# Kernel tuning notes

Hardware: AMD Instinct MI355X
Metric: run time of the kernel (lower is better)

Reference implementation:

```python
import jax, jax.numpy as jnp
import numpy as np

PRUNING_THRESHOLD = 0.02


def setup_inputs() -> dict:
    key = jax.random.key(0)
    ks = jax.random.split(key, 9)
    B, T, D = 2, 2048, 512
    H, S = 8, 16
    hd = D // H
    x = jax.random.normal(ks[0], (B, T, D), dtype=jnp.float32)
    Wqkv = jax.random.normal(ks[1], (3 * D, D), dtype=jnp.float32) * 0.02
    Wout = jax.random.normal(ks[2], (D, D), dtype=jnp.float32) * 0.02
    splat_centers = jax.random.normal(ks[3], (H, S, hd), dtype=jnp.float32) * 0.3
    splat_deltas = jax.random.normal(ks[4], (H, S, hd), dtype=jnp.float32) * 0.05
    splat_log_scales = jax.random.normal(ks[5], (H, S), dtype=jnp.float32) * 0.2 + jnp.float32(np.log(0.5))
    splat_log_amplitudes = jax.random.normal(ks[6], (H, S), dtype=jnp.float32) * 0.1 - 0.5
    movement_scale = jnp.float32(0.08)
    temperature = jnp.float32(1.0)
    return {"x": x, "Wqkv": Wqkv, "Wout": Wout,
            "splat_centers": splat_centers, "splat_deltas": splat_deltas,
            "splat_log_scales": splat_log_scales, "splat_log_amplitudes": splat_log_amplitudes,
            "movement_scale": movement_scale, "temperature": temperature}


def reference(x, Wqkv, Wout, splat_centers, splat_deltas,
              splat_log_scales, splat_log_amplitudes, movement_scale, temperature):
    B, T, D = x.shape
    H, S, hd = splat_centers.shape
    # qkv projection (nn.Linear: y = x @ W.T), split into q,k,v per head
    qkv = (x @ Wqkv.T).reshape(B, T, 3, H, hd)
    q, k, v = qkv[:, :, 0], qkv[:, :, 1], qkv[:, :, 2]  # [B,T,H,hd]
    # effective centers with bounded movement (eval mode: no warmup)
    bounded_scale = jax.nn.sigmoid(movement_scale) * 0.2
    centers = splat_centers + splat_deltas * bounded_scale  # [H,S,hd]
    scales = jnp.clip(jnp.exp(splat_log_scales), 0.01, 2.0)  # [H,S]
    amplitudes = jnp.clip(jnp.exp(splat_log_amplitudes), 1e-06, 10.0)
    amplitudes = amplitudes * (amplitudes > PRUNING_THRESHOLD).astype(amplitudes.dtype)
    # squared distances from tokens to splat centers: [B,T,H,S]
    q_dists = jnp.sum((q[:, :, :, None, :] - centers[None, None]) ** 2, axis=-1)
    k_dists = jnp.sum((k[:, :, :, None, :] - centers[None, None]) ** 2, axis=-1)
    inv_var = 1.0 / (scales ** 2 + 1e-08)  # [H,S]
    q_w = jnp.exp(-0.5 * q_dists * inv_var)  # [B,T,H,S]
    k_w = jnp.exp(-0.5 * k_dists * inv_var)
    # per-head splat-weighted logits: [B,T(query i),T(key j),H]
    logits = jnp.einsum('bihs,bjhs,hs->bijh', q_w, k_w, amplitudes)
    temp = jnp.clip(temperature, 0.1, 10.0)
    # NOTE: original vectorized path softmaxes over dim=1 (query axis) -- faithful
    attn = jax.nn.softmax(logits / temp, axis=1)
    out = jnp.einsum('btjh,bjhd->bthd', attn, v).reshape(B, T, D)
    return out @ Wout.T
```

## Files before the change

### kernel.cpp

```cpp
#include <hip/hip_runtime.h>
#include <hip/hip_bf16.h>
#include <hip/hip_fp16.h>
#include <cstdint>
#include <cstddef>

#define T_SEQ 2048
#define NBATCH 2
#define DIMD 512
#define NH 8
#define NS 16
#define HD 64
#define NBH 16

using s16x8 = __attribute__((ext_vector_type(8))) short;
using f32x4 = __attribute__((ext_vector_type(4))) float;

static __device__ inline unsigned short f2bf(float f) {
  __hip_bfloat16 h = __float2bfloat16(f);
  return reinterpret_cast<unsigned short&>(h);
}
static __device__ inline unsigned short f2h(float f) {
  __half h = __float2half(f);
  return reinterpret_cast<unsigned short&>(h);
}
static __device__ inline float h2f(unsigned short u) {
  __half h = reinterpret_cast<__half&>(u);
  return __half2float(h);
}
static __device__ inline unsigned int pack2(float a, float b) {
  return (unsigned int)f2bf(a) | ((unsigned int)f2bf(b) << 16);
}
static __device__ inline void gload16(const void* g, void* l) {
  __builtin_amdgcn_global_load_lds((const __attribute__((address_space(1))) void*)g,
                                   (__attribute__((address_space(3))) void*)l, 16, 0, 0);
}
static __device__ inline int swz_id() {
  int nwg = gridDim.x * gridDim.y;
  int orig = blockIdx.y * gridDim.x + blockIdx.x;
  return (orig & 7) * (nwg >> 3) + (orig >> 3);
}

static const size_t OFF_VBUF = 0;
static const size_t OFF_AOUT = 2097152;
static const size_t OFF_XH   = 6291456;
static const size_t OFF_WQH  = 8388608;
static const size_t OFF_WOH  = 9175040;
static const size_t OFF_QABF = 9437184;
static const size_t OFF_KWBF = 9961472;
static const size_t OFF_SPART= 10485760;
static const size_t OFF_VPART= 10616832;
static const size_t OFF_CADJ = 10633216;
static const size_t OFF_IVAR = 10641408;
static const size_t OFF_AMPT = 10641536;

__global__ __launch_bounds__(256) void prep(
    const float* __restrict__ x, const float* __restrict__ Wqkv, const float* __restrict__ Wout,
    const float* __restrict__ centers, const float* __restrict__ deltas,
    const float* __restrict__ lsc, const float* __restrict__ lam,
    const float* __restrict__ ms, const float* __restrict__ tp,
    unsigned short* __restrict__ xh, unsigned short* __restrict__ wqh,
    unsigned short* __restrict__ woh,
    float* __restrict__ cadj, float* __restrict__ ivar, float* __restrict__ ampt) {
  int bid = blockIdx.x;
  int tid = threadIdx.x;
  if (bid == 3072) {
    float bscale = 0.2f / (1.0f + expf(-ms[0]));
    float tclip = fminf(fmaxf(tp[0], 0.1f), 10.0f);
    if (tid < NH * NS) {
      float sc = fminf(fmaxf(expf(lsc[tid]), 0.01f), 2.0f);
      ivar[tid] = 1.0f / (sc * sc + 1e-8f);
      float am = fminf(fmaxf(expf(lam[tid]), 1e-6f), 10.0f);
      am = (am > 0.02f) ? am : 0.0f;
      ampt[tid] = am / tclip;
    }
    for (int e = tid; e < NH * NS * HD; e += 256)
      cadj[e] = centers[e] + deltas[e] * bscale;
    return;
  }
  const float* src; unsigned short* dh; int i4;
  if (bid < 2048)      { src = x;    dh = xh;  i4 = bid * 256 + tid; }
  else if (bid < 2816) { src = Wqkv; dh = wqh; i4 = (bid - 2048) * 256 + tid; }
  else                 { src = Wout; dh = woh; i4 = (bid - 2816) * 256 + tid; }
  float4 v = *(const float4*)&src[(size_t)i4 * 4];
  ushort4 hh;
  hh.x = f2h(v.x); hh.y = f2h(v.y); hh.z = f2h(v.z); hh.w = f2h(v.w);
  *(ushort4*)&dh[(size_t)i4 * 4] = hh;
}

template<int BM, int BN>
__device__ __forceinline__ void gemm_core(
    const unsigned short* Ah, const unsigned short* Bh,
    int K, int m0, int n0,
    unsigned short* ash, unsigned short* bsh,
    f32x4 (&acc)[BM / 32][BN / 32]) {
  constexpr int WM = BM / 2, WN = BN / 2;
  constexpr int MF = WM / 16, NF = WN / 16;
  constexpr int NSA = BM / 8, NSB = BN / 8;
  constexpr int TSEG = NSA + NSB;
  int tid = threadIdx.x;
  int w = tid >> 6, l = tid & 63, lm = l & 15, lq = l >> 4;
  int wm = w >> 1, wn = w & 1;
  int r8 = l >> 3, c8 = l & 7;
  int ksl = (c8 ^ (r8 & 7)) << 3;
#pragma unroll
  for (int mi = 0; mi < MF; ++mi)
#pragma unroll
    for (int ni = 0; ni < NF; ++ni) acc[mi][ni] = (f32x4){0.f, 0.f, 0.f, 0.f};

  for (int k0 = 0; k0 < K; k0 += 64) {
    __syncthreads();
#pragma unroll
    for (int t = 0; t < TSEG / 4; ++t) {
      int s = w + t * 4;
      if (s < NSA) {
        gload16(&Ah[(size_t)(m0 + s * 8 + r8) * K + k0 + ksl], &ash[s * 512]);
      } else {
        int ss = s - NSA;
        gload16(&Bh[(size_t)(n0 + ss * 8 + r8) * K + k0 + ksl], &bsh[ss * 512]);
      }
    }
    __syncthreads();
#pragma unroll
    for (int kh = 0; kh < 2; ++kh) {
      s16x8 fah[MF], fbh[NF];
#pragma unroll
      for (int mi = 0; mi < MF; ++mi) {
        int rr = wm * WM + mi * 16 + lm;
        int off = rr * 64 + ((((kh << 2) | lq) ^ (rr & 7)) << 3);
        fah[mi] = *(const s16x8*)&ash[off];
      }
#pragma unroll
      for (int ni = 0; ni < NF; ++ni) {
        int cc = wn * WN + ni * 16 + lm;
        int off = cc * 64 + ((((kh << 2) | lq) ^ (cc & 7)) << 3);
        fbh[ni] = *(const s16x8*)&bsh[off];
      }
#pragma unroll
      for (int mi = 0; mi < MF; ++mi)
#pragma unroll
        for (int ni = 0; ni < NF; ++ni)
          acc[mi][ni] = __builtin_amdgcn_mfma_f32_16x16x32_f16(fah[mi], fbh[ni], acc[mi][ni], 0, 0, 0);
    }
  }
}

template<int BM, int BN>
__device__ __forceinline__ void write_c(
    float* C, int ldc, int m0, int n0, f32x4 (&acc)[BM / 32][BN / 32]) {
  constexpr int WM = BM / 2, WN = BN / 2;
  int tid = threadIdx.x;
  int w = tid >> 6, l = tid & 63, lm = l & 15, lq = l >> 4;
  int wm = w >> 1, wn = w & 1;
#pragma unroll
  for (int mi = 0; mi < BM / 32; ++mi)
#pragma unroll
    for (int ni = 0; ni < BN / 32; ++ni)
#pragma unroll
      for (int r = 0; r < 4; ++r) {
        int row = m0 + wm * WM + mi * 16 + lq * 4 + r;
        int col = n0 + wn * WN + ni * 16 + lm;
        C[(size_t)row * ldc + col] = acc[mi][ni][r];
      }
}

template<int BM, int BN>
__device__ __forceinline__ void write_ch(
    unsigned short* C, int ldc, int m0, int n0, f32x4 (&acc)[BM / 32][BN / 32]) {
  constexpr int WM = BM / 2, WN = BN / 2;
  int tid = threadIdx.x;
  int w = tid >> 6, l = tid & 63, lm = l & 15, lq = l >> 4;
  int wm = w >> 1, wn = w & 1;
#pragma unroll
  for (int mi = 0; mi < BM / 32; ++mi)
#pragma unroll
    for (int ni = 0; ni < BN / 32; ++ni)
#pragma unroll
      for (int r = 0; r < 4; ++r) {
        int row = m0 + wm * WM + mi * 16 + lq * 4 + r;
        int col = n0 + wn * WN + ni * 16 + lm;
        C[(size_t)row * ldc + col] = f2h(acc[mi][ni][r]);
      }
}

__global__ __launch_bounds__(256) void gemm_qkv(
    const unsigned short* __restrict__ xh, const unsigned short* __restrict__ wqh,
    const float* __restrict__ cadj, const float* __restrict__ ivar,
    const float* __restrict__ ampt, unsigned short* __restrict__ vbuf,
    unsigned short* __restrict__ qa_bf, unsigned short* __restrict__ kw_bf) {
  __shared__ __align__(16) char smem[39168];
  unsigned short* ash = (unsigned short*)smem;
  unsigned short* bsh = (unsigned short*)(smem + 16384);
  int sid = swz_id();
  int bx = sid % 24, by = sid / 24;
  int m0 = by * 128;
  int tid = threadIdx.x;
  f32x4 acc[4][2];
  if (bx >= 16) {
    gemm_core<128, 64>(xh, wqh + (size_t)(1024 + (bx - 16) * 64) * 512,
                       512, m0, 0, ash, bsh, acc);
    write_ch<128, 64>(vbuf, 512, m0, (bx - 16) * 64, acc);
    return;
  }
  bool isk = bx >= 8;
  int h = bx & 7;
  gemm_core<128, 64>(xh, wqh + (size_t)((isk ? 512 : 0) + h * 64) * 512,
                     512, m0, 0, ash, bsh, acc);
  __syncthreads();
  float* q_s = (float*)smem;
  float* c_s = (float*)(smem + 34816);
  {
    int w = tid >> 6, l = tid & 63, lm = l & 15, lq = l >> 4;
    int wm = w >> 1, wn = w & 1;
#pragma unroll
    for (int mi = 0; mi < 4; ++mi)
#pragma unroll
      for (int ni = 0; ni < 2; ++ni)
#pragma unroll
        for (int r = 0; r < 4; ++r)
          q_s[(wm * 64 + mi * 16 + lq * 4 + r) * 68 + wn * 32 + ni * 16 + lm] = acc[mi][ni][r];
    int cr = tid >> 4, d4 = tid & 15;
    *(float4*)&c_s[cr * 68 + d4 * 4] = *(const float4*)&cadj[(h * 16 + cr) * 64 + d4 * 4];
  }
  __syncthreads();
  int s = tid & 15, rbase = tid >> 4;
  float iv = ivar[h * 16 + s];
  float am = ampt[h * 16 + s];
  const float4* crow = (const float4*)&c_s[s * 68];
#pragma unroll
  for (int t = 0; t < 8; ++t) {
    int r = t * 16 + rbase;
    const float4* qrow = (const float4*)&q_s[r * 68];
    float d2 = 0.0f;
#pragma unroll
    for (int d4 = 0; d4 < 16; ++d4) {
      float4 qv = qrow[d4], cv = crow[d4];
      float e0 = qv.x - cv.x, e1 = qv.y - cv.y, e2 = qv.z - cv.z, e3 = qv.w - cv.w;
      d2 = fmaf(e0, e0, d2); d2 = fmaf(e1, e1, d2);
      d2 = fmaf(e2, e2, d2); d2 = fmaf(e3, e3, d2);
    }
    float val = __expf(-0.5f * d2 * iv);
    int row = m0 + r;
    int b = row >> 11, i = row & 2047;
    size_t base = ((size_t)(b * 8 + h) * T_SEQ + i) * 32;
    if (!isk) {
      qa_bf[base + s] = f2bf(val * am);
      qa_bf[base + 16 + s] = 0;
    } else {
      int xorv = (r >> 1) & 3;
      int slot = s >> 3, e = s & 7;
      kw_bf[base + (size_t)((slot ^ xorv) << 3) + e] = f2bf(val);
      kw_bf[base + (size_t)(((2 + slot) ^ xorv) << 3) + e] = 0;
    }
  }
}

__global__ __launch_bounds__(256) void gemm_out(
    const unsigned short* __restrict__ aout_h, const unsigned short* __restrict__ woh,
    float* __restrict__ out) {
  __shared__ __align__(16) unsigned short ash[64 * 64];
  __shared__ __align__(16) unsigned short bsh[64 * 64];
  int sid = swz_id();
  int bx = sid % 8, by = sid / 8;
  f32x4 acc[2][2];
  gemm_core<64, 64>(aout_h + (size_t)by * 64 * 512, woh + (size_t)bx * 64 * 512,
                    512, 0, 0, ash, bsh, acc);
  write_c<64, 64>(out, 512, by * 64, bx * 64, acc);
}

__global__ __launch_bounds__(256) void k3_colsum(
    const unsigned short* __restrict__ qa_bf, const unsigned short* __restrict__ kw_bf,
    float* __restrict__ spart) {
  int sid = swz_id();
  int jblk = sid & 15, yy = sid >> 4;
  int bh = yy >> 2, iq = yy & 3;
  int tid = threadIdx.x;
  int w = tid >> 6, l = tid & 63, lm = l & 15, lq = l >> 4;
  int jbase = (jblk << 7) + (w << 5);
  int sw = lq ^ ((lm >> 1) & 3);
  size_t base32 = (size_t)bh * T_SEQ * 32;
  s16x8 kwB0 = *(const s16x8*)&kw_bf[base32 + (size_t)(jbase + lm) * 32 + sw * 8];
  s16x8 kwB1 = *(const s16x8*)&kw_bf[base32 + (size_t)(jbase + 16 + lm) * 32 + sw * 8];
  const unsigned short* qp = qa_bf + base32 + ((size_t)(iq * 512) + lm) * 32 + lq * 8;
  float s0 = 0.0f, s1 = 0.0f;
  f32x4 z = (f32x4){0.f, 0.f, 0.f, 0.f};
#pragma unroll 4
  for (int it = 0; it < 512; it += 16) {
    s16x8 qaA = *(const s16x8*)(qp + (size_t)it * 32);
    f32x4 L0 = __builtin_amdgcn_mfma_f32_16x16x32_bf16(qaA, kwB0, z, 0, 0, 0);
    f32x4 L1 = __builtin_amdgcn_mfma_f32_16x16x32_bf16(qaA, kwB1, z, 0, 0, 0);
    s0 += (__expf(L0[0]) - 1.0f) + (__expf(L0[1]) - 1.0f)
        + (__expf(L0[2]) - 1.0f) + (__expf(L0[3]) - 1.0f);
    s1 += (__expf(L1[0]) - 1.0f) + (__expf(L1[1]) - 1.0f)
        + (__expf(L1[2]) - 1.0f) + (__expf(L1[3]) - 1.0f);
  }
  s0 += __shfl_xor(s0, 16); s0 += __shfl_xor(s0, 32);
  s1 += __shfl_xor(s1, 16); s1 += __shfl_xor(s1, 32);
  if (l < 16) {
    float* sp = spart + ((size_t)iq * NBH + bh) * T_SEQ;
    sp[jbase + lm] = s0;
    sp[jbase + 16 + lm] = s1;
  }
}

__global__ __launch_bounds__(256) void k3c_vt(
    const unsigned short* __restrict__ vbuf, const float* __restrict__ spart,
    unsigned short* __restrict__ vt, float* __restrict__ vpart) {
  int bh = blockIdx.y; int b = bh >> 3, h = bh & 7;
  int js = blockIdx.x << 7;
  int tid = threadIdx.x;
  __shared__ unsigned short t_s[64][136];
  __shared__ float red[16][64];
  int jg = tid >> 4, dq = tid & 15;
  const unsigned short* vb = vbuf + (size_t)b * T_SEQ * 512 + h * 64;
  const float* sp0 = spart + (size_t)bh * T_SEQ + js;
  const float* sp1 = spart + ((size_t)NBH + bh) * T_SEQ + js;
  const float* sp2 = spart + ((size_t)2 * NBH + bh) * T_SEQ + js;
  const float* sp3 = spart + ((size_t)3 * NBH + bh) * T_SEQ + js;
  float a0 = 0.f, a1 = 0.f, a2 = 0.f, a3 = 0.f;
#pragma unroll
  for (int p = 0; p < 8; ++p) {
    int j = p * 16 + jg;
    float s = 1.0f / (2048.0f + sp0[j] + sp1[j] + sp2[j] + sp3[j]);
    ushort4 vu = *(const ushort4*)&vb[(size_t)(js + j) * 512 + dq * 4];
    float v0 = h2f(vu.x) * s, v1 = h2f(vu.y) * s, v2 = h2f(vu.z) * s, v3 = h2f(vu.w) * s;
    t_s[dq * 4 + 0][j] = f2bf(v0);
    t_s[dq * 4 + 1][j] = f2bf(v1);
    t_s[dq * 4 + 2][j] = f2bf(v2);
    t_s[dq * 4 + 3][j] = f2bf(v3);
    a0 += v0; a1 += v1; a2 += v2; a3 += v3;
  }
  red[jg][dq * 4 + 0] = a0; red[jg][dq * 4 + 1] = a1;
  red[jg][dq * 4 + 2] = a2; red[jg][dq * 4 + 3] = a3;
  __syncthreads();
  if (tid < 64) {
    float t = 0.f;
#pragma unroll
    for (int g = 0; g < 16; ++g) t += red[g][tid];
    vpart[((size_t)blockIdx.x * NBH + bh) * 64 + tid] = t;
  }
#pragma unroll
  for (int p = 0; p < 4; ++p) {
    int idx = p * 256 + tid;
    int d = idx >> 4, seg = idx & 15;
    int4 val = *(const int4*)&t_s[d][seg * 8];
    int col = ((seg >> 3) << 6) + ((((seg & 7) ^ (d & 7))) << 3);
    *(int4*)&vt[(size_t)bh * 131072 + (size_t)d * 2048 + js + col] = val;
  }
}

__global__ __launch_bounds__(512) void k4_attnout(
    const unsigned short* __restrict__ qa_bf, const unsigned short* __restrict__ kw_bf,
    const unsigned short* __restrict__ vt, const float* __restrict__ vpart,
    unsigned short* __restrict__ aout_h) {
  int sid = swz_id();
  int bh = sid >> 4; int b = bh >> 3, h = bh & 7;
  int i0 = (sid & 15) << 7;
  int tid = threadIdx.x;
  int w = tid >> 6, l = tid & 63, lm = l & 15, lq = l >> 4;
  int ig = w >> 1, jh = w & 1;
  __shared__ __align__(16) unsigned short kwS[2][2][2048];
  __shared__ __align__(16) unsigned short vtS[2][2][4096];
  const unsigned short* kwg = kw_bf + (size_t)bh * (T_SEQ * 32) + (size_t)jh * (1024 * 32);
  const unsigned short* vtg = vt + (size_t)bh * 131072 + jh * 1024;
  int p0 = ((lm >> 2) << 3) | (lm & 3);
  int sw0 = lq ^ ((lm >> 1) & 1);
  int sw1 = sw0 ^ 2;
  int swv = lm & 7;
  s16x8 qaB0 = *(const s16x8*)&qa_bf[((size_t)bh * T_SEQ + i0 + ig * 32 + lm) * 32 + lq * 8];
  s16x8 qaB1 = *(const s16x8*)&qa_bf[((size_t)bh * T_SEQ + i0 + ig * 32 + 16 + lm) * 32 + lq * 8];
  f32x4 acc[2][4];
#pragma unroll
  for (int ifr = 0; ifr < 2; ++ifr)
#pragma unroll
    for (int df = 0; df < 4; ++df) acc[ifr][df] = (f32x4){0.f, 0.f, 0.f, 0.f};
  f32x4 z = (f32x4){0.f, 0.f, 0.f, 0.f};

  auto stage = [&](int c, int bsel) {
#pragma unroll
    for (int t = 0; t < 2; ++t) {
      int li = ig * 2 + t;
      gload16(&vtg[(size_t)(li * 8 + (l >> 3)) * 2048 + c * 64 + (l & 7) * 8],
              &vtS[jh][bsel][li * 512]);
    }
    gload16(&kwg[(size_t)(c * 64 + ig * 16 + (l >> 2)) * 32 + (l & 3) * 8],
            &kwS[jh][bsel][ig * 512]);
  };

  stage(0, 0);
  __syncthreads();
  for (int c = 0; c < 16; ++c) {
    int bsel = c & 1;
    if (c < 15) stage(c + 1, bsel ^ 1);
    const unsigned short* kwb = kwS[jh][bsel];
    const unsigned short* vtb = vtS[jh][bsel];
#pragma unroll
    for (int s = 0; s < 2; ++s) {
      s16x8 ka0 = *(const s16x8*)&kwb[(s * 32 + p0) * 32 + sw0 * 8];
      s16x8 ka1 = *(const s16x8*)&kwb[(s * 32 + p0 + 4) * 32 + sw1 * 8];
      s16x8 vb0 = *(const s16x8*)&vtb[(size_t)(0 + lm) * 64 + (((4 * s + lq) ^ swv) << 3)];
      s16x8 vb1 = *(const s16x8*)&vtb[(size_t)(16 + lm) * 64 + (((4 * s + lq) ^ swv) << 3)];
      s16x8 vb2 = *(const s16x8*)&vtb[(size_t)(32 + lm) * 64 + (((4 * s + lq) ^ swv) << 3)];
      s16x8 vb3 = *(const s16x8*)&vtb[(size_t)(48 + lm) * 64 + (((4 * s + lq) ^ swv) << 3)];
#pragma unroll
      for (int ifr = 0; ifr < 2; ++ifr) {
        s16x8 qaB = ifr ? qaB1 : qaB0;
        f32x4 L0 = __builtin_amdgcn_mfma_f32_16x16x32_bf16(ka0, qaB, z, 0, 0, 0);
        f32x4 L1 = __builtin_amdgcn_mfma_f32_16x16x32_bf16(ka1, qaB, z, 0, 0, 0);
        union { unsigned int u4[4]; s16x8 v; } cvt;
        cvt.u4[0] = pack2(__expf(L0[0]) - 1.0f, __expf(L0[1]) - 1.0f);
        cvt.u4[1] = pack2(__expf(L0[2]) - 1.0f, __expf(L0[3]) - 1.0f);
        cvt.u4[2] = pack2(__expf(L1[0]) - 1.0f, __expf(L1[1]) - 1.0f);
        cvt.u4[3] = pack2(__expf(L1[2]) - 1.0f, __expf(L1[3]) - 1.0f);
        s16x8 pA = cvt.v;
        __builtin_amdgcn_s_setprio(1);
        acc[ifr][0] = __builtin_amdgcn_mfma_f32_16x16x32_bf16(pA, vb0, acc[ifr][0], 0, 0, 0);
        acc[ifr][1] = __builtin_amdgcn_mfma_f32_16x16x32_bf16(pA, vb1, acc[ifr][1], 0, 0, 0);
        acc[ifr][2] = __builtin_amdgcn_mfma_f32_16x16x32_bf16(pA, vb2, acc[ifr][2], 0, 0, 0);
        acc[ifr][3] = __builtin_amdgcn_mfma_f32_16x16x32_bf16(pA, vb3, acc[ifr][3], 0, 0, 0);
        __builtin_amdgcn_s_setprio(0);
      }
    }
    __syncthreads();
  }
  float* mrg = (float*)&vtS[0][0][0];
  if (jh == 1) {
#pragma unroll
    for (int ifr = 0; ifr < 2; ++ifr)
#pragma unroll
      for (int df = 0; df < 4; ++df)
#pragma unroll
        for (int r = 0; r < 4; ++r)
          mrg[(((ig * 2 + ifr) * 4 + df) * 4 + r) * 64 + l] = acc[ifr][df][r];
  }
  __syncthreads();
  if (jh == 0) {
#pragma unroll
    for (int ifr = 0; ifr < 2; ++ifr)
#pragma unroll
      for (int df = 0; df < 4; ++df) {
        int d = df * 16 + lm;
        float vs = 0.0f;
#pragma unroll
        for (int js = 0; js < 16; ++js) vs += vpart[((size_t)js * NBH + bh) * 64 + d];
#pragma unroll
        for (int r = 0; r < 4; ++r) {
          int row = i0 + ig * 32 + ifr * 16 + lq * 4 + r;
          float o = acc[ifr][df][r] + mrg[(((ig * 2 + ifr) * 4 + df) * 4 + r) * 64 + l] + vs;
          aout_h[((size_t)b * T_SEQ + row) * DIMD + h * 64 + d] = f2h(o);
        }
      }
  }
}

extern "C" void kernel_launch(void* const* d_in, const int* in_sizes, int n_in,
                              void* d_out, int out_size, void* d_ws, size_t ws_size,
                              hipStream_t stream) {
  const float* x    = (const float*)d_in[0];
  const float* Wqkv = (const float*)d_in[1];
  const float* Wout = (const float*)d_in[2];
  const float* ctr  = (const float*)d_in[3];
  const float* dlt  = (const float*)d_in[4];
  const float* lsc  = (const float*)d_in[5];
  const float* lam  = (const float*)d_in[6];
  const float* ms   = (const float*)d_in[7];
  const float* tp   = (const float*)d_in[8];
  float* ws = (float*)d_ws;
  unsigned short* vbuf   = (unsigned short*)(ws + OFF_VBUF);
  unsigned short* aout_h = (unsigned short*)(ws + OFF_AOUT);
  unsigned short* xh  = (unsigned short*)(ws + OFF_XH);
  unsigned short* wqh = (unsigned short*)(ws + OFF_WQH);
  unsigned short* woh = (unsigned short*)(ws + OFF_WOH);
  unsigned short* qa_bf = (unsigned short*)(ws + OFF_QABF);
  unsigned short* kw_bf = (unsigned short*)(ws + OFF_KWBF);
  float* spart = ws + OFF_SPART;
  float* vpart = ws + OFF_VPART;
  float* cadj  = ws + OFF_CADJ;
  float* ivar  = ws + OFF_IVAR;
  float* ampt  = ws + OFF_AMPT;
  unsigned short* vt = xh;
  float* out = (float*)d_out;

  prep<<<3073, 256, 0, stream>>>(x, Wqkv, Wout, ctr, dlt, lsc, lam, ms, tp,
                                 xh, wqh, woh, cadj, ivar, ampt);
  gemm_qkv<<<dim3(24, 32), 256, 0, stream>>>(xh, wqh, cadj, ivar, ampt,
                                             vbuf, qa_bf, kw_bf);
  k3_colsum<<<dim3(16, 64), 256, 0, stream>>>(qa_bf, kw_bf, spart);
  k3c_vt<<<dim3(16, 16), 256, 0, stream>>>(vbuf, spart, vt, vpart);
  k4_attnout<<<dim3(16, 16), 512, 0, stream>>>(qa_bf, kw_bf, vt, vpart, aout_h);
  gemm_out<<<dim3(8, 64), 256, 0, stream>>>(aout_h, woh, out);
}
```

Baseline: 84.11 us.

## Split attention-output key range across four wave groups per block

```diff
diff --git a/kernel.cpp b/kernel.cpp
--- a/kernel.cpp
+++ b/kernel.cpp
@@ -348,7 +348,7 @@
   }
 }
 
-__global__ __launch_bounds__(512) void k4_attnout(
+__global__ __launch_bounds__(1024) void k4_attnout(
     const unsigned short* __restrict__ qa_bf, const unsigned short* __restrict__ kw_bf,
     const unsigned short* __restrict__ vt, const float* __restrict__ vpart,
     unsigned short* __restrict__ aout_h) {
@@ -357,11 +357,13 @@
   int i0 = (sid & 15) << 7;
   int tid = threadIdx.x;
   int w = tid >> 6, l = tid & 63, lm = l & 15, lq = l >> 4;
-  int ig = w >> 1, jh = w & 1;
-  __shared__ __align__(16) unsigned short kwS[2][2][2048];
-  __shared__ __align__(16) unsigned short vtS[2][2][4096];
-  const unsigned short* kwg = kw_bf + (size_t)bh * (T_SEQ * 32) + (size_t)jh * (1024 * 32);
-  const unsigned short* vtg = vt + (size_t)bh * 131072 + jh * 1024;
+  int ig = w >> 2, jq = w & 3;
+  __shared__ __align__(16) char smem[98304];
+  unsigned short* kwS = (unsigned short*)smem;
+  unsigned short* vtS = (unsigned short*)(smem + 32768);
+  float* mrg = (float*)smem;
+  const unsigned short* kwg = kw_bf + (size_t)bh * (T_SEQ * 32) + (size_t)jq * (512 * 32);
+  const unsigned short* vtg = vt + (size_t)bh * 131072 + jq * 512;
   int p0 = ((lm >> 2) << 3) | (lm & 3);
   int sw0 = lq ^ ((lm >> 1) & 1);
   int sw1 = sw0 ^ 2;
@@ -380,19 +382,19 @@
     for (int t = 0; t < 2; ++t) {
       int li = ig * 2 + t;
       gload16(&vtg[(size_t)(li * 8 + (l >> 3)) * 2048 + c * 64 + (l & 7) * 8],
-              &vtS[jh][bsel][li * 512]);
+              &vtS[(jq * 2 + bsel) * 4096 + li * 512]);
     }
     gload16(&kwg[(size_t)(c * 64 + ig * 16 + (l >> 2)) * 32 + (l & 3) * 8],
-            &kwS[jh][bsel][ig * 512]);
+            &kwS[(jq * 2 + bsel) * 2048 + ig * 512]);
   };
 
   stage(0, 0);
   __syncthreads();
-  for (int c = 0; c < 16; ++c) {
+  for (int c = 0; c < 8; ++c) {
     int bsel = c & 1;
-    if (c < 15) stage(c + 1, bsel ^ 1);
-    const unsigned short* kwb = kwS[jh][bsel];
-    const unsigned short* vtb = vtS[jh][bsel];
+    if (c < 7) stage(c + 1, bsel ^ 1);
+    const unsigned short* kwb = &kwS[(jq * 2 + bsel) * 2048];
+    const unsigned short* vtb = &vtS[(jq * 2 + bsel) * 4096];
 #pragma unroll
     for (int s = 0; s < 2; ++s) {
       s16x8 ka0 = *(const s16x8*)&kwb[(s * 32 + p0) * 32 + sw0 * 8];
@@ -422,18 +424,18 @@
     }
     __syncthreads();
   }
-  float* mrg = (float*)&vtS[0][0][0];
-  if (jh == 1) {
+  if (jq != 0) {
+    int base = ((jq - 1) * 4 + ig) * 2;
 #pragma unroll
     for (int ifr = 0; ifr < 2; ++ifr)
 #pragma unroll
       for (int df = 0; df < 4; ++df)
 #pragma unroll
         for (int r = 0; r < 4; ++r)
-          mrg[(((ig * 2 + ifr) * 4 + df) * 4 + r) * 64 + l] = acc[ifr][df][r];
+          mrg[(((base + ifr) * 4 + df) * 4 + r) * 64 + l] = acc[ifr][df][r];
   }
   __syncthreads();
-  if (jh == 0) {
+  if (jq == 0) {
 #pragma unroll
     for (int ifr = 0; ifr < 2; ++ifr)
 #pragma unroll
@@ -445,7 +447,10 @@
 #pragma unroll
         for (int r = 0; r < 4; ++r) {
           int row = i0 + ig * 32 + ifr * 16 + lq * 4 + r;
-          float o = acc[ifr][df][r] + mrg[(((ig * 2 + ifr) * 4 + df) * 4 + r) * 64 + l] + vs;
+          float o = acc[ifr][df][r] + vs;
+#pragma unroll
+          for (int jm = 0; jm < 3; ++jm)
+            o += mrg[((((jm * 4 + ig) * 2 + ifr) * 4 + df) * 4 + r) * 64 + l];
           aout_h[((size_t)b * T_SEQ + row) * DIMD + h * 64 + d] = f2h(o);
         }
       }
@@ -486,6 +491,6 @@
                                              vbuf, qa_bf, kw_bf);
   k3_colsum<<<dim3(16, 64), 256, 0, stream>>>(qa_bf, kw_bf, spart);
   k3c_vt<<<dim3(16, 16), 256, 0, stream>>>(vbuf, spart, vt, vpart);
-  k4_attnout<<<dim3(16, 16), 512, 0, stream>>>(qa_bf, kw_bf, vt, vpart, aout_h);
+  k4_attnout<<<dim3(16, 16), 1024, 0, stream>>>(qa_bf, kw_bf, vt, vpart, aout_h);
   gemm_out<<<dim3(8, 64), 256, 0, stream>>>(aout_h, woh, out);
 }
```

Measured after the change: 79.44 us. 5.6% less time.
